# Kernel tuning notes

Hardware: AMD Instinct MI355X
Metric: run time of the kernel (lower is better)

The kernel has to match this reference:

```python
import jax, jax.numpy as jnp
import numpy as np

KEY_CHANNELS = 256


def conv1x1_relu(x, w, b):
    # x: [B, Cin, H, W], w: [Cout, Cin], b: [Cout] -> [B, Cout, H, W]
    y = jnp.einsum('oc,bchw->bohw', w, x) + b[None, :, None, None]
    return jax.nn.relu(y)


def setup_inputs() -> dict:
    key = jax.random.key(0)
    ks = jax.random.split(key, 16)
    B, C, H, W = 8, 512, 128, 128
    Kc, Kp = KEY_CHANNELS, 150
    sc = lambda cin: 1.0 / np.sqrt(cin)
    return {
        'x': jax.random.normal(ks[0], (B, C, H, W), jnp.float32),
        'proxy': jax.random.normal(ks[1], (B, C, Kp, 1), jnp.float32),
        'w_fp1': jax.random.normal(ks[2], (Kc, C), jnp.float32) * sc(C),
        'b_fp1': jax.random.normal(ks[3], (Kc,), jnp.float32) * 0.1,
        'w_fp2': jax.random.normal(ks[4], (Kc, Kc), jnp.float32) * sc(Kc),
        'b_fp2': jax.random.normal(ks[5], (Kc,), jnp.float32) * 0.1,
        'w_fo1': jax.random.normal(ks[6], (Kc, C), jnp.float32) * sc(C),
        'b_fo1': jax.random.normal(ks[7], (Kc,), jnp.float32) * 0.1,
        'w_fo2': jax.random.normal(ks[8], (Kc, Kc), jnp.float32) * sc(Kc),
        'b_fo2': jax.random.normal(ks[9], (Kc,), jnp.float32) * 0.1,
        'w_fd': jax.random.normal(ks[10], (Kc, C), jnp.float32) * sc(C),
        'b_fd': jax.random.normal(ks[11], (Kc,), jnp.float32) * 0.1,
        'w_fu': jax.random.normal(ks[12], (C, Kc), jnp.float32) * sc(Kc),
        'b_fu': jax.random.normal(ks[13], (C,), jnp.float32) * 0.1,
    }


def reference(x, proxy, w_fp1, b_fp1, w_fp2, b_fp2, w_fo1, b_fo1,
              w_fo2, b_fo2, w_fd, b_fd, w_fu, b_fu):
    B, C, H, W = x.shape
    Kc = w_fp1.shape[0]
    # f_pixel: two 1x1 conv(+folded BN)+ReLU blocks -> query [B, HW, Kc]
    q = conv1x1_relu(conv1x1_relu(x, w_fp1, b_fp1), w_fp2, b_fp2)
    query = q.reshape(B, Kc, H * W).transpose(0, 2, 1)
    # f_object -> key [B, Kc, Kp]
    k = conv1x1_relu(conv1x1_relu(proxy, w_fo1, b_fo1), w_fo2, b_fo2)
    key = k.reshape(B, Kc, -1)
    # f_down -> value [B, Kp, Kc]
    v = conv1x1_relu(proxy, w_fd, b_fd)
    value = v.reshape(B, Kc, -1).transpose(0, 2, 1)
    # cross-attention: softmax(Q K^T / sqrt(Kc)) V
    sim = jnp.einsum('bnc,bck->bnk', query, key) * (Kc ** -0.5)
    sim = jax.nn.softmax(sim, axis=-1)
    context = jnp.einsum('bnk,bkc->bnc', sim, value)  # [B, HW, Kc]
    context = context.transpose(0, 2, 1).reshape(B, Kc, H, W)
    # f_up: 1x1 conv(+folded BN)+ReLU back to in_channels
    return conv1x1_relu(context, w_fu, b_fu)
```

## Files before the change

### kernel.cpp

```cpp
#include <hip/hip_runtime.h>
#include <hip/hip_bf16.h>


typedef __bf16 bf16x8 __attribute__((ext_vector_type(8)));
typedef float f32x4 __attribute__((ext_vector_type(4)));

#define AS1 __attribute__((address_space(1)))
#define AS3 __attribute__((address_space(3)))
#define MFMA_16x16x32(a, b, c) __builtin_amdgcn_mfma_f32_16x16x32_bf16((a), (b), (c), 0, 0, 0)

__device__ __forceinline__ unsigned short f2bf(float f) {
  union { float f; unsigned u; } x; x.f = f;
  unsigned r = (x.u + 0x7FFFu + ((x.u >> 16) & 1u)) >> 16;
  return (unsigned short)r;
}

__global__ __launch_bounds__(256) void kv_kernel(
    const float* __restrict__ proxy,
    const float* __restrict__ w_fo1, const float* __restrict__ b_fo1,
    const float* __restrict__ w_fo2, const float* __restrict__ b_fo2,
    const float* __restrict__ w_fd, const float* __restrict__ b_fd,
    unsigned short* __restrict__ keyT, unsigned short* __restrict__ Vv,
    const float* __restrict__ w1, const float* __restrict__ w2,
    const float* __restrict__ wu, unsigned short* __restrict__ W1b,
    unsigned short* __restrict__ W2b, unsigned short* __restrict__ Wub) {
  __shared__ float cols[512][8];
  __shared__ float k1s[256][8];
  const int b = blockIdx.y;
  const int p0 = blockIdx.x * 8;
  const int t = threadIdx.x;
  {
    const int base = ((b * 20 + blockIdx.x) * 256 + t) * 8;
#pragma unroll
    for (int i = 0; i < 8; i++) {
      const int idx = base + i;
      if (idx < 131072) W1b[idx] = f2bf(w1[idx]);
      else if (idx < 196608) W2b[idx - 131072] = f2bf(w2[idx - 131072]);
      else Wub[idx - 196608] = f2bf(wu[idx - 196608]);
    }
  }
#pragma unroll
  for (int i = 0; i < 8; i++) {
    int idx = t + i * 256;
    int c = idx >> 2, q = idx & 3;
    int p = p0 + q * 2;
    float2 v = make_float2(0.f, 0.f);
    if (p < 150) v = *(const float2*)(proxy + ((size_t)b * 512 + c) * 150 + p);
    cols[c][q * 2 + 0] = v.x;
    cols[c][q * 2 + 1] = v.y;
  }
  __syncthreads();
  float accV[8], accK[8];
  {
    float bv = b_fd[t], bk = b_fo1[t];
#pragma unroll
    for (int px = 0; px < 8; px++) { accV[px] = bv; accK[px] = bk; }
  }
#define KV_FMA(j, wv_, wk_)                                      \
  { float4 ca = *(const float4*)&cols[c + j][0];                 \
    float4 cb = *(const float4*)&cols[c + j][4];                 \
    accV[0] += wv_ * ca.x; accV[1] += wv_ * ca.y;                \
    accV[2] += wv_ * ca.z; accV[3] += wv_ * ca.w;                \
    accV[4] += wv_ * cb.x; accV[5] += wv_ * cb.y;                \
    accV[6] += wv_ * cb.z; accV[7] += wv_ * cb.w;                \
    accK[0] += wk_ * ca.x; accK[1] += wk_ * ca.y;                \
    accK[2] += wk_ * ca.z; accK[3] += wk_ * ca.w;                \
    accK[4] += wk_ * cb.x; accK[5] += wk_ * cb.y;                \
    accK[6] += wk_ * cb.z; accK[7] += wk_ * cb.w; }
  for (int c = 0; c < 512; c += 4) {
    float4 wv4 = *(const float4*)(w_fd + (size_t)t * 512 + c);
    float4 wk4 = *(const float4*)(w_fo1 + (size_t)t * 512 + c);
    KV_FMA(0, wv4.x, wk4.x)
    KV_FMA(1, wv4.y, wk4.y)
    KV_FMA(2, wv4.z, wk4.z)
    KV_FMA(3, wv4.w, wk4.w)
  }
#pragma unroll
  for (int px = 0; px < 8; px++) {
    Vv[((size_t)b * 256 + t) * 160 + p0 + px] = f2bf(fmaxf(accV[px], 0.f));
    k1s[t][px] = fmaxf(accK[px], 0.f);
  }
  __syncthreads();
  float accY[8];
  {
    float by = b_fo2[t];
#pragma unroll
    for (int px = 0; px < 8; px++) accY[px] = by;
  }
#define KV_FMA2(j, wy_)                                          \
  { float4 ca = *(const float4*)&k1s[c + j][0];                  \
    float4 cb = *(const float4*)&k1s[c + j][4];                  \
    accY[0] += wy_ * ca.x; accY[1] += wy_ * ca.y;                \
    accY[2] += wy_ * ca.z; accY[3] += wy_ * ca.w;                \
    accY[4] += wy_ * cb.x; accY[5] += wy_ * cb.y;                \
    accY[6] += wy_ * cb.z; accY[7] += wy_ * cb.w; }
  for (int c = 0; c < 256; c += 4) {
    float4 wy4 = *(const float4*)(w_fo2 + (size_t)t * 256 + c);
    KV_FMA2(0, wy4.x)
    KV_FMA2(1, wy4.y)
    KV_FMA2(2, wy4.z)
    KV_FMA2(3, wy4.w)
  }
#pragma unroll
  for (int px = 0; px < 8; px++)
    keyT[((size_t)b * 160 + p0 + px) * 256 + t] = f2bf(fmaxf(accY[px], 0.f));
}

__global__ __launch_bounds__(256, 3) void gemm1_fused(
    const float* __restrict__ X, const unsigned short* __restrict__ Bt,
    const float* __restrict__ bias, unsigned short* __restrict__ Cq) {
  const int HW = 16384, K = 512, N = 256;
  __shared__ float Af[64 * 128];
  __shared__ unsigned short Bs[128 * 64];
  const int r = blockIdx.x;
  const int b = blockIdx.y;
  const int my = ((r >> 4) << 3) | (r & 7);
  const int nx = (r >> 3) & 1;
  const int m0 = my * 128, n0 = nx * 128;
  const int tid = threadIdx.x;
  const int w = tid >> 6, l = tid & 63;
  const int lr = l & 15, lg = l >> 4;
  const int wm = (w >> 1) * 64, wn = (w & 1) * 64;
  const float* Xb = X + (size_t)b * K * HW;
  const unsigned short* Btb = Bt + (size_t)n0 * K;
  const f32x4 zero = {0.f, 0.f, 0.f, 0.f};
  f32x4 acc[4][4];
#pragma unroll
  for (int m = 0; m < 4; m++)
#pragma unroll
    for (int n = 0; n < 4; n++) acc[m][n] = zero;

  const int arow = l >> 5, acol = l & 31;
  const int bsub = l >> 3, bcol = (l & 7) * 8;
  for (int kt = 0; kt < K; kt += 64) {
    __syncthreads();
#pragma unroll
    for (int i = 0; i < 8; i++) {
      const int rk = w * 16 + i * 2 + arow;
      const int s = (rk >> 3) & 7;
      __builtin_amdgcn_global_load_lds(
          (AS1 void*)(Xb + (size_t)(kt + rk) * HW + m0 + ((acol ^ s) << 2)),
          (AS3 void*)(Af + (w * 16 + i * 2) * 128), 16, 0, 0);
    }
#pragma unroll
    for (int i = 0; i < 4; i++) {
      __builtin_amdgcn_global_load_lds(
          (AS1 void*)(Btb + (size_t)(w * 32 + i * 8 + bsub) * K + kt + bcol),
          (AS3 void*)(Bs + (w * 32 + i * 8) * 64), 16, 0, 0);
    }
    __syncthreads();
#pragma unroll
    for (int ks = 0; ks < 2; ks++) {
      bf16x8 aF[4], bF[4];
      const int s = ks * 4 + lg;
#pragma unroll
      for (int m = 0; m < 4; m++) {
        const int p = wm + m * 16 + lr;
        const int cb = ((((p >> 2) ^ s) << 2) | (p & 3));
        bf16x8 a;
#pragma unroll
        for (int j = 0; j < 8; j++)
          a[j] = (__bf16)Af[(ks * 32 + lg * 8 + j) * 128 + cb];
        aF[m] = a;
      }
#pragma unroll
      for (int n = 0; n < 4; n++)
        bF[n] = *(const bf16x8*)(Bs + (wn + n * 16 + lr) * 64 + ks * 32 + lg * 8);
#pragma unroll
      for (int m = 0; m < 4; m++)
#pragma unroll
        for (int n = 0; n < 4; n++) acc[m][n] = MFMA_16x16x32(aF[m], bF[n], acc[m][n]);
    }
  }
  unsigned short* Cb = Cq + (size_t)b * HW * N;
#pragma unroll
  for (int m = 0; m < 4; m++) {
#pragma unroll
    for (int n = 0; n < 4; n++) {
      const int col = n0 + wn + n * 16 + lr;
      const float bc = bias[col];
#pragma unroll
      for (int r2 = 0; r2 < 4; r2++) {
        const int row = m0 + wm + m * 16 + lg * 4 + r2;
        Cb[(size_t)row * N + col] = f2bf(fmaxf(acc[m][n][r2] + bc, 0.f));
      }
    }
  }
}

template <int BIAS_ROW, int OUTF32, int COLOC, int KC>
__global__ __launch_bounds__(256, 4) void gemm_bt_relu(
    const unsigned short* __restrict__ A, const unsigned short* __restrict__ Bt,
    const float* __restrict__ bias, void* __restrict__ Cout,
    int M, int N, long long sA, long long sB, long long sC) {
  __shared__ unsigned short As[128 * 64];
  __shared__ unsigned short Bs[128 * 64];
  int m0, n0, b;
  if (COLOC == 1) {
    const int g = blockIdx.x, x = g & 7, j = g >> 3;
    const int og = ((j >> 1) << 3) | x;
    n0 = (j & 1) * 128; m0 = (og & 127) * 128; b = og >> 7;
  } else if (COLOC == 2) {
    const int g = blockIdx.x, x = g & 7, j = g >> 3;
    const int og = ((j >> 2) << 3) | x;
    m0 = (j & 3) * 128; n0 = (og & 127) * 128; b = og >> 7;
  } else {
    b = blockIdx.z; m0 = blockIdx.x * 128; n0 = blockIdx.y * 128;
  }
  const int tid = threadIdx.x;
  const int w = tid >> 6, l = tid & 63;
  const int lr = l & 15, lg = l >> 4;
  const int wm = (w >> 1) * 64, wn = (w & 1) * 64;
  const unsigned short* Ab = A + (size_t)b * sA + (size_t)m0 * KC;
  const unsigned short* Btb = Bt + (size_t)b * sB + (size_t)n0 * KC;
  const f32x4 zero = {0.f, 0.f, 0.f, 0.f};
  f32x4 acc[4][4];
#pragma unroll
  for (int m = 0; m < 4; m++)
#pragma unroll
    for (int n = 0; n < 4; n++) acc[m][n] = zero;

  const int srow = w * 32 + (l >> 3);
  const int scol = (l & 7) * 8;
#pragma unroll
  for (int kt = 0; kt < KC; kt += 64) {
    __syncthreads();
#pragma unroll
    for (int i = 0; i < 4; i++) {
      __builtin_amdgcn_global_load_lds(
          (AS1 void*)(Ab + (size_t)(srow + i * 8) * KC + kt + scol),
          (AS3 void*)(As + (w * 32 + i * 8) * 64), 16, 0, 0);
      __builtin_amdgcn_global_load_lds(
          (AS1 void*)(Btb + (size_t)(srow + i * 8) * KC + kt + scol),
          (AS3 void*)(Bs + (w * 32 + i * 8) * 64), 16, 0, 0);
    }
    __syncthreads();
#pragma unroll
    for (int ks = 0; ks < 2; ks++) {
      bf16x8 aF[4], bF[4];
#pragma unroll
      for (int m = 0; m < 4; m++)
        aF[m] = *(const bf16x8*)(As + (wm + m * 16 + lr) * 64 + ks * 32 + lg * 8);
#pragma unroll
      for (int n = 0; n < 4; n++)
        bF[n] = *(const bf16x8*)(Bs + (wn + n * 16 + lr) * 64 + ks * 32 + lg * 8);
#pragma unroll
      for (int m = 0; m < 4; m++)
#pragma unroll
        for (int n = 0; n < 4; n++) acc[m][n] = MFMA_16x16x32(aF[m], bF[n], acc[m][n]);
    }
  }
#pragma unroll
  for (int m = 0; m < 4; m++) {
#pragma unroll
    for (int n = 0; n < 4; n++) {
      const int col = n0 + wn + n * 16 + lr;
      const float bc = BIAS_ROW ? 0.f : bias[col];
#pragma unroll
      for (int r = 0; r < 4; r++) {
        const int row = m0 + wm + m * 16 + lg * 4 + r;
        float v = acc[m][n][r] + (BIAS_ROW ? bias[row] : bc);
        v = fmaxf(v, 0.f);
        if (OUTF32)
          ((float*)Cout)[(size_t)b * sC + (size_t)row * N + col] = v;
        else
          ((unsigned short*)Cout)[(size_t)b * sC + (size_t)row * N + col] = f2bf(v);
      }
    }
  }
}

__global__ __launch_bounds__(256, 4) void attn_kernel(
    const unsigned short* __restrict__ Q, const unsigned short* __restrict__ Kt,
    const unsigned short* __restrict__ Vv, unsigned short* __restrict__ ctxT) {
  const int HW = 16384;
  __shared__ unsigned short Pls[128 * 160];
  const int b = blockIdx.y;
  const int pix0 = blockIdx.x * 128;
  const int tid = threadIdx.x;
  const int w = tid >> 6, l = tid & 63;
  const int lr = l & 15, lg = l >> 4;
  const unsigned short* Qb = Q + ((size_t)b * HW + pix0 + w * 32) * 256;
  const unsigned short* Kb = Kt + (size_t)b * 160 * 256;
  const unsigned short* Vb = Vv + (size_t)b * 256 * 160;
  const f32x4 zero = {0.f, 0.f, 0.f, 0.f};

  f32x4 acc[2][10];
#pragma unroll
  for (int m = 0; m < 2; m++)
#pragma unroll
    for (int n = 0; n < 10; n++) acc[m][n] = zero;
#pragma unroll 2
  for (int ks = 0; ks < 8; ks++) {
    bf16x8 aF[2];
#pragma unroll
    for (int m = 0; m < 2; m++)
      aF[m] = *(const bf16x8*)(Qb + (size_t)(m * 16 + lr) * 256 + ks * 32 + lg * 8);
    __builtin_amdgcn_s_setprio(1);
#pragma unroll
    for (int n = 0; n < 10; n++) {
      bf16x8 bF = *(const bf16x8*)(Kb + (size_t)(n * 16 + lr) * 256 + ks * 32 + lg * 8);
      acc[0][n] = MFMA_16x16x32(aF[0], bF, acc[0][n]);
      acc[1][n] = MFMA_16x16x32(aF[1], bF, acc[1][n]);
    }
    __builtin_amdgcn_s_setprio(0);
  }
  const float scale = 0.0625f;
#pragma unroll
  for (int m = 0; m < 2; m++) {
#pragma unroll
    for (int r = 0; r < 4; r++) {
      float lm = -1e30f;
#pragma unroll
      for (int n = 0; n < 10; n++) {
        float v = acc[m][n][r] * scale;
        acc[m][n][r] = v;
        if (n * 16 + lr < 150) lm = fmaxf(lm, v);
      }
#pragma unroll
      for (int msk = 1; msk <= 8; msk <<= 1) lm = fmaxf(lm, __shfl_xor(lm, msk, 64));
      float s = 0.f;
#pragma unroll
      for (int n = 0; n < 10; n++) {
        float p = (n * 16 + lr < 150) ? __expf(acc[m][n][r] - lm) : 0.f;
        acc[m][n][r] = p;
        s += p;
      }
#pragma unroll
      for (int msk = 1; msk <= 8; msk <<= 1) s += __shfl_xor(s, msk, 64);
      float inv = 1.f / s;
      const int row = w * 32 + m * 16 + lg * 4 + r;
      const unsigned sw = (unsigned)(row & 7) << 4;
#pragma unroll
      for (int n = 0; n < 10; n++) {
        unsigned boff = (unsigned)row * 320 + (unsigned)(n * 16 + lr) * 2;
        *(unsigned short*)((char*)Pls + (boff ^ sw)) = f2bf(acc[m][n][r] * inv);
      }
    }
  }
  unsigned short* Cb = ctxT + ((size_t)b * HW + pix0 + w * 32) * 256;
#pragma unroll
  for (int half = 0; half < 2; half++) {
    f32x4 acc2[2][8];
#pragma unroll
    for (int m = 0; m < 2; m++)
#pragma unroll
      for (int n = 0; n < 8; n++) acc2[m][n] = zero;
    for (int ks = 0; ks < 5; ks++) {
      bf16x8 aP[2];
#pragma unroll
      for (int m = 0; m < 2; m++) {
        const int row = w * 32 + m * 16 + lr;
        unsigned boff = (unsigned)row * 320 + (unsigned)(ks * 64 + lg * 16);
        aP[m] = *(const bf16x8*)((const char*)Pls + (boff ^ ((unsigned)(row & 7) << 4)));
      }
      __builtin_amdgcn_s_setprio(1);
#pragma unroll
      for (int n = 0; n < 8; n++) {
        const int ch = half * 128 + n * 16 + lr;
        bf16x8 bV = *(const bf16x8*)(Vb + (size_t)ch * 160 + ks * 32 + lg * 8);
        acc2[0][n] = MFMA_16x16x32(aP[0], bV, acc2[0][n]);
        acc2[1][n] = MFMA_16x16x32(aP[1], bV, acc2[1][n]);
      }
      __builtin_amdgcn_s_setprio(0);
    }
#pragma unroll
    for (int m = 0; m < 2; m++)
#pragma unroll
      for (int n = 0; n < 8; n++)
#pragma unroll
        for (int r = 0; r < 4; r++)
          Cb[(size_t)(m * 16 + lg * 4 + r) * 256 + half * 128 + n * 16 + lr] =
              f2bf(acc2[m][n][r]);
  }
}

extern "C" void kernel_launch(void* const* d_in, const int* in_sizes, int n_in,
                              void* d_out, int out_size, void* d_ws, size_t ws_size,
                              hipStream_t stream) {
  (void)in_sizes; (void)n_in; (void)out_size;
  const float* x     = (const float*)d_in[0];
  const float* proxy = (const float*)d_in[1];
  const float* w_fp1 = (const float*)d_in[2];
  const float* b_fp1 = (const float*)d_in[3];
  const float* w_fp2 = (const float*)d_in[4];
  const float* b_fp2 = (const float*)d_in[5];
  const float* w_fo1 = (const float*)d_in[6];
  const float* b_fo1 = (const float*)d_in[7];
  const float* w_fo2 = (const float*)d_in[8];
  const float* b_fo2 = (const float*)d_in[9];
  const float* w_fd  = (const float*)d_in[10];
  const float* b_fd  = (const float*)d_in[11];
  const float* w_fu  = (const float*)d_in[12];
  const float* b_fu  = (const float*)d_in[13];

  char* ws = (char*)d_ws;
  unsigned short* W1b  = (unsigned short*)(ws + 0);
  unsigned short* W2b  = (unsigned short*)(ws + 262144);
  unsigned short* Wub  = (unsigned short*)(ws + 393216);
  unsigned short* keyT = (unsigned short*)(ws + 655360);
  unsigned short* Vv   = (unsigned short*)(ws + 1310720);
  unsigned short* bufA = (unsigned short*)(ws + 2097152);
  unsigned short* bufB = (unsigned short*)(ws + 2097152 + 134217728);
  if (ws_size < 203423744) return;

  dim3 blk(256);
  kv_kernel<<<dim3(20, 8), blk, 0, stream>>>(proxy, w_fo1, b_fo1, w_fo2, b_fo2,
                                             w_fd, b_fd, keyT, Vv,
                                             w_fp1, w_fp2, w_fu, W1b, W2b, Wub);
  gemm1_fused<<<dim3(256, 8), blk, 0, stream>>>(x, W1b, b_fp1, bufB);
  gemm_bt_relu<0, 0, 1, 256><<<2048, blk, 0, stream>>>(
      bufB, W2b, b_fp2, bufA, 16384, 256,
      (long long)16384 * 256, 0, (long long)16384 * 256);
  attn_kernel<<<dim3(128, 8), blk, 0, stream>>>(bufA, keyT, Vv, bufB);
  gemm_bt_relu<1, 1, 2, 256><<<4096, blk, 0, stream>>>(
      Wub, bufB, b_fu, d_out, 512, 16384,
      0, (long long)16384 * 256, (long long)512 * 16384);
}
```

Measured before the change: 359.1 us.

## Convert X tile to bf16 in registers and store transposed swizzled LDS

In gemm1, the A operand (the fp32 X tile) is now loaded into registers with float4 global loads and converted to bf16 before it reaches LDS. It is written in a transposed, XOR-swizzled [pixel][k] layout, so each MFMA A fragment is one 16-byte LDS read instead of eight scalar fp32 reads plus conversions. The bf16 tile halves the LDS footprint, and launch bounds are raised to 4 blocks per CU for more occupancy. The cost is that the direct global-to-LDS async load for A is replaced by synchronous register loads and strided LDS stores, which can reduce overlap and adds register pressure.

```diff
diff --git a/kernel.cpp b/kernel.cpp
--- a/kernel.cpp
+++ b/kernel.cpp
@@ -13,6 +13,12 @@
   union { float f; unsigned u; } x; x.f = f;
   unsigned r = (x.u + 0x7FFFu + ((x.u >> 16) & 1u)) >> 16;
   return (unsigned short)r;
+}
+
+__device__ __forceinline__ unsigned bfpack(float a, float b) {
+  union { __bf16 h; unsigned short u; } x, y;
+  x.h = (__bf16)a; y.h = (__bf16)b;
+  return (unsigned)x.u | ((unsigned)y.u << 16);
 }
 
 __global__ __launch_bounds__(256) void kv_kernel(
@@ -106,11 +112,11 @@
     keyT[((size_t)b * 160 + p0 + px) * 256 + t] = f2bf(fmaxf(accY[px], 0.f));
 }
 
-__global__ __launch_bounds__(256, 3) void gemm1_fused(
+__global__ __launch_bounds__(256, 4) void gemm1_fused(
     const float* __restrict__ X, const unsigned short* __restrict__ Bt,
     const float* __restrict__ bias, unsigned short* __restrict__ Cq) {
   const int HW = 16384, K = 512, N = 256;
-  __shared__ float Af[64 * 128];
+  __shared__ __align__(16) unsigned short Afb[128 * 64];
   __shared__ unsigned short Bs[128 * 64];
   const int r = blockIdx.x;
   const int b = blockIdx.y;
@@ -130,38 +136,48 @@
 #pragma unroll
     for (int n = 0; n < 4; n++) acc[m][n] = zero;
 
-  const int arow = l >> 5, acol = l & 31;
+  const int q = tid >> 3, jp = tid & 7;
+  const float* Xq = Xb + m0 + q * 4;
   const int bsub = l >> 3, bcol = (l & 7) * 8;
   for (int kt = 0; kt < K; kt += 64) {
     __syncthreads();
-#pragma unroll
-    for (int i = 0; i < 8; i++) {
-      const int rk = w * 16 + i * 2 + arow;
-      const int s = (rk >> 3) & 7;
-      __builtin_amdgcn_global_load_lds(
-          (AS1 void*)(Xb + (size_t)(kt + rk) * HW + m0 + ((acol ^ s) << 2)),
-          (AS3 void*)(Af + (w * 16 + i * 2) * 128), 16, 0, 0);
-    }
 #pragma unroll
     for (int i = 0; i < 4; i++) {
       __builtin_amdgcn_global_load_lds(
           (AS1 void*)(Btb + (size_t)(w * 32 + i * 8 + bsub) * K + kt + bcol),
           (AS3 void*)(Bs + (w * 32 + i * 8) * 64), 16, 0, 0);
     }
+#pragma unroll
+    for (int c = 0; c < 2; c++) {
+      const int kr = 4 * jp + 32 * c;
+      float4 v0 = *(const float4*)(Xq + (size_t)(kt + kr + 0) * HW);
+      float4 v1 = *(const float4*)(Xq + (size_t)(kt + kr + 1) * HW);
+      float4 v2 = *(const float4*)(Xq + (size_t)(kt + kr + 2) * HW);
+      float4 v3 = *(const float4*)(Xq + (size_t)(kt + kr + 3) * HW);
+#pragma unroll
+      for (int e = 0; e < 4; e++) {
+        const int p = q * 4 + e;
+        const float a0 = e == 0 ? v0.x : e == 1 ? v0.y : e == 2 ? v0.z : v0.w;
+        const float a1 = e == 0 ? v1.x : e == 1 ? v1.y : e == 2 ? v1.z : v1.w;
+        const float a2 = e == 0 ? v2.x : e == 1 ? v2.y : e == 2 ? v2.z : v2.w;
+        const float a3 = e == 0 ? v3.x : e == 1 ? v3.y : e == 2 ? v3.z : v3.w;
+        const unsigned boff =
+            ((unsigned)p * 128 + (unsigned)jp * 8 + (unsigned)c * 64) ^
+            (((unsigned)p & 7u) << 4);
+        uint2 pk = make_uint2(bfpack(a0, a1), bfpack(a2, a3));
+        *(uint2*)((char*)Afb + boff) = pk;
+      }
+    }
     __syncthreads();
 #pragma unroll
     for (int ks = 0; ks < 2; ks++) {
       bf16x8 aF[4], bF[4];
-      const int s = ks * 4 + lg;
 #pragma unroll
       for (int m = 0; m < 4; m++) {
         const int p = wm + m * 16 + lr;
-        const int cb = ((((p >> 2) ^ s) << 2) | (p & 3));
-        bf16x8 a;
-#pragma unroll
-        for (int j = 0; j < 8; j++)
-          a[j] = (__bf16)Af[(ks * 32 + lg * 8 + j) * 128 + cb];
-        aF[m] = a;
+        const unsigned boff = ((unsigned)p * 128 + (unsigned)(ks * 64 + lg * 16)) ^
+                              (((unsigned)p & 7u) << 4);
+        aF[m] = *(const bf16x8*)((const char*)Afb + boff);
       }
 #pragma unroll
       for (int n = 0; n < 4; n++)
```

After: 373.5 us. 1.04x slower.

## Restructure attention kernel: transposed MFMA, register-shuffled P, LDS-staged coalesced output

Applied to the files above, without the earlier changes.

The attention kernel now computes S^T = K·Q^T with 16 pixels per wave and 64 pixels per block, doubling the grid. Softmax probabilities move between lanes with wave shuffles into MFMA B-operand layout instead of going through LDS. The context tile is staged in a swizzled LDS buffer so the output can be written with 16-byte coalesced stores instead of scattered 2-byte stores. The cost is more shuffles and fewer MFMAs per K/V fragment load, which lowers reuse of K and V.

```diff
diff --git a/kernel.cpp b/kernel.cpp
--- a/kernel.cpp
+++ b/kernel.cpp
@@ -13,6 +13,10 @@
   union { float f; unsigned u; } x; x.f = f;
   unsigned r = (x.u + 0x7FFFu + ((x.u >> 16) & 1u)) >> 16;
   return (unsigned short)r;
+}
+
+__device__ __forceinline__ unsigned bfpack(float a, float b) {
+  return (unsigned)f2bf(a) | ((unsigned)f2bf(b) << 16);
 }
 
 __global__ __launch_bounds__(256) void kv_kernel(
@@ -274,104 +278,126 @@
     const unsigned short* __restrict__ Q, const unsigned short* __restrict__ Kt,
     const unsigned short* __restrict__ Vv, unsigned short* __restrict__ ctxT) {
   const int HW = 16384;
-  __shared__ unsigned short Pls[128 * 160];
+  __shared__ __align__(16) char ctx_lds[65 * 512];
   const int b = blockIdx.y;
-  const int pix0 = blockIdx.x * 128;
-  const int tid = threadIdx.x;
+  const int pix0 = blockIdx.x * 64;
+  const int tid = (int)threadIdx.x;
   const int w = tid >> 6, l = tid & 63;
-  const int lr = l & 15, lg = l >> 4;
-  const unsigned short* Qb = Q + ((size_t)b * HW + pix0 + w * 32) * 256;
+  const int lr = l & 15, lg = (l >> 4) & 3;
+  const int pixb = pix0 + w * 16;
+  const unsigned short* Qb = Q + ((size_t)b * HW + pixb) * 256;
   const unsigned short* Kb = Kt + (size_t)b * 160 * 256;
   const unsigned short* Vb = Vv + (size_t)b * 256 * 160;
   const f32x4 zero = {0.f, 0.f, 0.f, 0.f};
 
-  f32x4 acc[2][10];
-#pragma unroll
-  for (int m = 0; m < 2; m++)
-#pragma unroll
-    for (int n = 0; n < 10; n++) acc[m][n] = zero;
+  f32x4 acc[10];
+#pragma unroll
+  for (int n = 0; n < 10; n++) acc[n] = zero;
 #pragma unroll 2
   for (int ks = 0; ks < 8; ks++) {
-    bf16x8 aF[2];
-#pragma unroll
-    for (int m = 0; m < 2; m++)
-      aF[m] = *(const bf16x8*)(Qb + (size_t)(m * 16 + lr) * 256 + ks * 32 + lg * 8);
+    bf16x8 bQ = *(const bf16x8*)(Qb + (size_t)lr * 256 + ks * 32 + lg * 8);
     __builtin_amdgcn_s_setprio(1);
 #pragma unroll
     for (int n = 0; n < 10; n++) {
-      bf16x8 bF = *(const bf16x8*)(Kb + (size_t)(n * 16 + lr) * 256 + ks * 32 + lg * 8);
-      acc[0][n] = MFMA_16x16x32(aF[0], bF, acc[0][n]);
-      acc[1][n] = MFMA_16x16x32(aF[1], bF, acc[1][n]);
+      bf16x8 aK = *(const bf16x8*)(Kb + (size_t)(n * 16 + lr) * 256 + ks * 32 + lg * 8);
+      acc[n] = MFMA_16x16x32(aK, bQ, acc[n]);
     }
     __builtin_amdgcn_s_setprio(0);
   }
   const float scale = 0.0625f;
-#pragma unroll
-  for (int m = 0; m < 2; m++) {
+  const int kof = lg << 2;
+  float mx = -1e30f;
+#pragma unroll
+  for (int n = 0; n < 10; n++)
 #pragma unroll
     for (int r = 0; r < 4; r++) {
-      float lm = -1e30f;
-#pragma unroll
-      for (int n = 0; n < 10; n++) {
-        float v = acc[m][n][r] * scale;
-        acc[m][n][r] = v;
-        if (n * 16 + lr < 150) lm = fmaxf(lm, v);
-      }
-#pragma unroll
-      for (int msk = 1; msk <= 8; msk <<= 1) lm = fmaxf(lm, __shfl_xor(lm, msk, 64));
-      float s = 0.f;
-#pragma unroll
-      for (int n = 0; n < 10; n++) {
-        float p = (n * 16 + lr < 150) ? __expf(acc[m][n][r] - lm) : 0.f;
-        acc[m][n][r] = p;
-        s += p;
-      }
-#pragma unroll
-      for (int msk = 1; msk <= 8; msk <<= 1) s += __shfl_xor(s, msk, 64);
-      float inv = 1.f / s;
-      const int row = w * 32 + m * 16 + lg * 4 + r;
-      const unsigned sw = (unsigned)(row & 7) << 4;
-#pragma unroll
-      for (int n = 0; n < 10; n++) {
-        unsigned boff = (unsigned)row * 320 + (unsigned)(n * 16 + lr) * 2;
-        *(unsigned short*)((char*)Pls + (boff ^ sw)) = f2bf(acc[m][n][r] * inv);
-      }
-    }
-  }
-  unsigned short* Cb = ctxT + ((size_t)b * HW + pix0 + w * 32) * 256;
+      float v = acc[n][r] * scale;
+      v = (n * 16 + kof + r < 150) ? v : -1e30f;
+      acc[n][r] = v;
+      mx = fmaxf(mx, v);
+    }
+  mx = fmaxf(mx, __shfl_xor(mx, 16, 64));
+  mx = fmaxf(mx, __shfl_xor(mx, 32, 64));
+  float s = 0.f;
+#pragma unroll
+  for (int n = 0; n < 10; n++)
+#pragma unroll
+    for (int r = 0; r < 4; r++) {
+      float e = __expf(acc[n][r] - mx);
+      acc[n][r] = e;
+      s += e;
+    }
+  s += __shfl_xor(s, 16, 64);
+  s += __shfl_xor(s, 32, 64);
+  const float inv = 1.f / s;
+  unsigned d0[10], d1[10];
+#pragma unroll
+  for (int n = 0; n < 10; n++) {
+    d0[n] = bfpack(acc[n][0] * inv, acc[n][1] * inv);
+    d1[n] = bfpack(acc[n][2] * inv, acc[n][3] * inv);
+  }
+  const int srcA = lr + ((lg & 1) << 5);
+  const int srcB = srcA + 16;
+  const bool hi = (lg >> 1) != 0;
+  uint4 wv[5];
+#pragma unroll
+  for (int k2 = 0; k2 < 5; k2++) {
+    unsigned e0 = (unsigned)__shfl((int)d0[2 * k2], srcA);
+    unsigned e1 = (unsigned)__shfl((int)d1[2 * k2], srcA);
+    unsigned e2 = (unsigned)__shfl((int)d0[2 * k2], srcB);
+    unsigned e3 = (unsigned)__shfl((int)d1[2 * k2], srcB);
+    unsigned o0 = (unsigned)__shfl((int)d0[2 * k2 + 1], srcA);
+    unsigned o1 = (unsigned)__shfl((int)d1[2 * k2 + 1], srcA);
+    unsigned o2 = (unsigned)__shfl((int)d0[2 * k2 + 1], srcB);
+    unsigned o3 = (unsigned)__shfl((int)d1[2 * k2 + 1], srcB);
+    wv[k2].x = hi ? o0 : e0;
+    wv[k2].y = hi ? o1 : e1;
+    wv[k2].z = hi ? o2 : e2;
+    wv[k2].w = hi ? o3 : e3;
+  }
+  const int pixL = w * 16 + lr;
+  const unsigned swz = ((unsigned)pixL & 7u) << 4;
 #pragma unroll
   for (int half = 0; half < 2; half++) {
-    f32x4 acc2[2][8];
-#pragma unroll
-    for (int m = 0; m < 2; m++)
-#pragma unroll
-      for (int n = 0; n < 8; n++) acc2[m][n] = zero;
-    for (int ks = 0; ks < 5; ks++) {
-      bf16x8 aP[2];
-#pragma unroll
-      for (int m = 0; m < 2; m++) {
-        const int row = w * 32 + m * 16 + lr;
-        unsigned boff = (unsigned)row * 320 + (unsigned)(ks * 64 + lg * 16);
-        aP[m] = *(const bf16x8*)((const char*)Pls + (boff ^ ((unsigned)(row & 7) << 4)));
-      }
+    f32x4 acc2[8];
+#pragma unroll
+    for (int m = 0; m < 8; m++) acc2[m] = zero;
+#pragma unroll
+    for (int k2 = 0; k2 < 5; k2++) {
+      union { uint4 u; bf16x8 h; } cvt; cvt.u = wv[k2];
+      const bf16x8 bP = cvt.h;
       __builtin_amdgcn_s_setprio(1);
 #pragma unroll
-      for (int n = 0; n < 8; n++) {
-        const int ch = half * 128 + n * 16 + lr;
-        bf16x8 bV = *(const bf16x8*)(Vb + (size_t)ch * 160 + ks * 32 + lg * 8);
-        acc2[0][n] = MFMA_16x16x32(aP[0], bV, acc2[0][n]);
-        acc2[1][n] = MFMA_16x16x32(aP[1], bV, acc2[1][n]);
+      for (int m = 0; m < 8; m++) {
+        bf16x8 aV = *(const bf16x8*)(Vb + (size_t)(half * 128 + m * 16 + lr) * 160 +
+                                     k2 * 32 + lg * 8);
+        acc2[m] = MFMA_16x16x32(aV, bP, acc2[m]);
       }
       __builtin_amdgcn_s_setprio(0);
     }
 #pragma unroll
-    for (int m = 0; m < 2; m++)
-#pragma unroll
-      for (int n = 0; n < 8; n++)
-#pragma unroll
-        for (int r = 0; r < 4; r++)
-          Cb[(size_t)(m * 16 + lg * 4 + r) * 256 + half * 128 + n * 16 + lr] =
-              f2bf(acc2[m][n][r]);
+    for (int m = 0; m < 8; m++) {
+      uint2 v;
+      v.x = bfpack(acc2[m][0], acc2[m][1]);
+      v.y = bfpack(acc2[m][2], acc2[m][3]);
+      const unsigned boff =
+          ((unsigned)pixL * 512 + (unsigned)(half * 128 + m * 16 + lg * 4) * 2) ^ swz;
+      *(uint2*)(ctx_lds + boff) = v;
+    }
+  }
+  asm volatile("s_waitcnt lgkmcnt(0)" ::: "memory");
+  __builtin_amdgcn_sched_barrier(0);
+  {
+    const int prow = w * 16 + (l >> 2);
+    const int chunk = l & 3;
+    unsigned short* Ob = ctxT + ((size_t)b * HW + pix0 + prow) * 256 + chunk * 64;
+    const unsigned rswz = ((unsigned)prow & 7u) << 4;
+#pragma unroll
+    for (int i = 0; i < 8; i++) {
+      const unsigned boff = ((unsigned)prow * 512 + (unsigned)chunk * 128 + i * 16) ^ rswz;
+      uint4 v = *(const uint4*)(ctx_lds + boff);
+      *(uint4*)(Ob + i * 8) = v;
+    }
   }
 }
 
@@ -412,7 +438,7 @@
   gemm_bt_relu<0, 0, 1, 256><<<2048, blk, 0, stream>>>(
       bufB, W2b, b_fp2, bufA, 16384, 256,
       (long long)16384 * 256, 0, (long long)16384 * 256);
-  attn_kernel<<<dim3(128, 8), blk, 0, stream>>>(bufA, keyT, Vv, bufB);
+  attn_kernel<<<dim3(256, 8), blk, 0, stream>>>(bufA, keyT, Vv, bufB);
   gemm_bt_relu<1, 1, 2, 256><<<4096, blk, 0, stream>>>(
       Wub, bufB, b_fu, d_out, 512, 16384,
       0, (long long)16384 * 256, (long long)512 * 16384);
```

Measured after the change: 405.7 us. 13.0% more time.
